# Performance work log

Measured on AMD Instinct MI355X. Metric: run time of the kernel, lower is better.

Reference implementation:

```python
import jax, jax.numpy as jnp
import numpy as np

INPUT_DIM = 1024
OUT_DIM = 1024
ORDER = 4
EXPANSION_POINT = 0.0


def setup_inputs() -> dict:
    key = jax.random.key(0)
    k_x, k_c = jax.random.split(key)
    x = jax.random.normal(k_x, (8192, INPUT_DIM), dtype=jnp.float32)
    coeffs = jax.random.normal(k_c, (OUT_DIM, INPUT_DIM, ORDER), dtype=jnp.float32) * 0.01
    bias = jnp.zeros((1, OUT_DIM), dtype=jnp.float32)
    return {"x": x, "coeffs": coeffs, "bias": bias}


def reference(x, coeffs, bias):
    # x: [..., input_dim] -> flatten leading dims
    outshape = x.shape[:-1] + (OUT_DIM,)
    xf = x.reshape(-1, INPUT_DIM)
    x_shifted = xf - EXPANSION_POINT
    # powers P[n, i, k] = x_shifted^k, k = 0..order-1 (0**0 == 1, matching torch)
    powers = jnp.power(x_shifted[:, :, None], jnp.arange(ORDER, dtype=x.dtype))
    # y[n, o] = sum_{i,k} P[n,i,k] * coeffs[o,i,k]  -- single GEMM-like contraction
    y = jnp.einsum('nik,oik->no', powers, coeffs)
    y = y + bias
    return y.reshape(outshape)
```

## Files before the change

kernel.cpp:

```cpp
#include <hip/hip_runtime.h>
#include <stdint.h>

#define IN_DIM 1024
#define OUT_DIM 1024
#define NROWS 8192
#define KD 3072

#define BM 256
#define BN 128
#define BK 64
#define NT (KD / BK)

typedef __bf16 bf16x8 __attribute__((ext_vector_type(8)));
typedef float f32x4 __attribute__((ext_vector_type(4)));
typedef unsigned short us8 __attribute__((ext_vector_type(8)));
typedef unsigned int u32;

#define AS1 __attribute__((address_space(1)))
#define AS3 __attribute__((address_space(3)))

__device__ __forceinline__ unsigned short f2bf(float f) {
    u32 u = __builtin_bit_cast(u32, f);
    u32 r = (u + 0x7fffu + ((u >> 16) & 1u)) >> 16;
    return (unsigned short)r;
}

__device__ __forceinline__ bf16x8 ld8(const unsigned short* p) {
    return __builtin_bit_cast(bf16x8, *reinterpret_cast<const us8*>(p));
}

__global__ __launch_bounds__(256) void prep_coeffs(const float* __restrict__ c,
                                                   const float* __restrict__ bias,
                                                   unsigned short* __restrict__ B,
                                                   float* __restrict__ bias2) {
    const int o = blockIdx.x;
    const float4* row = reinterpret_cast<const float4*>(c + (size_t)o * (IN_DIM * 4));
    unsigned short* Bo = B + (size_t)o * KD;
    float s = 0.f;
    for (int i = threadIdx.x; i < IN_DIM; i += 256) {
        float4 v = row[i];
        s += v.x;
        Bo[i]        = f2bf(v.y);
        Bo[1024 + i] = f2bf(v.z);
        Bo[2048 + i] = f2bf(v.w);
    }
#pragma unroll
    for (int off = 32; off; off >>= 1) s += __shfl_down(s, off);
    __shared__ float red[4];
    if ((threadIdx.x & 63) == 0) red[threadIdx.x >> 6] = s;
    __syncthreads();
    if (threadIdx.x == 0) bias2[o] = bias[o] + red[0] + red[1] + red[2] + red[3];
}

__global__ __launch_bounds__(256) void prep_powers(const float* __restrict__ x,
                                                   unsigned short* __restrict__ A) {
    int t = blockIdx.x * blockDim.x + threadIdx.x;
    int n = t >> 8;
    int i4 = (t & 255) * 4;
    float4 v = reinterpret_cast<const float4*>(x)[t];
    unsigned short* An = A + (size_t)n * KD + i4;
    float xs[4] = {v.x, v.y, v.z, v.w};
    unsigned short b1[4], b2[4], b3[4];
#pragma unroll
    for (int j = 0; j < 4; ++j) {
        float x1 = xs[j], x2 = x1 * x1, x3 = x2 * x1;
        b1[j] = f2bf(x1); b2[j] = f2bf(x2); b3[j] = f2bf(x3);
    }
    ushort4 p1 = {b1[0], b1[1], b1[2], b1[3]};
    ushort4 p2 = {b2[0], b2[1], b2[2], b2[3]};
    ushort4 p3 = {b3[0], b3[1], b3[2], b3[3]};
    *reinterpret_cast<ushort4*>(An)        = p1;
    *reinterpret_cast<ushort4*>(An + 1024) = p2;
    *reinterpret_cast<ushort4*>(An + 2048) = p3;
}

__global__ __launch_bounds__(512, 2) void taylor_gemm(
    const unsigned short* __restrict__ A,
    const unsigned short* __restrict__ B,
    const float* __restrict__ bias2,
    float* __restrict__ C) {
    __shared__ alignas(16) unsigned short sA[3][BM * BK];
    __shared__ alignas(16) unsigned short sB[3][BN * BK];

    const int tid = threadIdx.x;
    const int lane = tid & 63;
    const int wid = tid >> 6;
    const int wr = wid >> 1;
    const int wc = wid & 1;
    const int gx = blockIdx.x, gy = blockIdx.y;

    const char* Ab = (const char*)A;
    const char* Bb = (const char*)B;
    const int cs = ((lane & 7) ^ (lane >> 3)) * 8;
    size_t aSrc[4], bSrc[2];
    int aDst[4], bDst[2];
#pragma unroll
    for (int u = 0; u < 4; ++u) {
        int row = gx * BM + u * 64 + wid * 8 + (lane >> 3);
        aSrc[u] = ((size_t)row * KD + cs) * 2;
        aDst[u] = (u * 64 + wid * 8) * BK;
    }
#pragma unroll
    for (int u = 0; u < 2; ++u) {
        int row = gy * BN + u * 64 + wid * 8 + (lane >> 3);
        bSrc[u] = ((size_t)row * KD + cs) * 2;
        bDst[u] = (u * 64 + wid * 8) * BK;
    }

    auto stage_all = [&](int b, int kt) {
        size_t koff = (size_t)kt * (BK * 2);
#pragma unroll
        for (int u = 0; u < 4; ++u)
            __builtin_amdgcn_global_load_lds(
                (const AS1 void*)(Ab + aSrc[u] + koff),
                (AS3 void*)(&sA[b][aDst[u]]), 16, 0, 0);
#pragma unroll
        for (int u = 0; u < 2; ++u)
            __builtin_amdgcn_global_load_lds(
                (const AS1 void*)(Bb + bSrc[u] + koff),
                (AS3 void*)(&sB[b][bDst[u]]), 16, 0, 0);
    };

    int aSw[2], bSw[2];
#pragma unroll
    for (int ks = 0; ks < 2; ++ks) {
        int sw = ((ks * 4 + (lane >> 4)) ^ (lane & 7)) * 8;
        aSw[ks] = (wr * 64 + (lane & 15)) * BK + sw;
        bSw[ks] = (wc * 64 + (lane & 15)) * BK + sw;
    }

    bf16x8 fa0[4][2], fb0[4][2], fa1[4][2], fb1[4][2];
    f32x4 acc[4][4] = {};

    auto read_frags = [&](bf16x8 (&fa)[4][2], bf16x8 (&fb)[4][2], int b) {
        const unsigned short* sAc = &sA[b][0];
        const unsigned short* sBc = &sB[b][0];
#pragma unroll
        for (int n = 0; n < 4; ++n)
#pragma unroll
            for (int ks = 0; ks < 2; ++ks)
                fb[n][ks] = ld8(&sBc[bSw[ks] + n * 16 * BK]);
#pragma unroll
        for (int m = 0; m < 4; ++m)
#pragma unroll
            for (int ks = 0; ks < 2; ++ks)
                fa[m][ks] = ld8(&sAc[aSw[ks] + m * 16 * BK]);
    };

    auto mfma_all = [&](bf16x8 (&fa)[4][2], bf16x8 (&fb)[4][2]) {
        __builtin_amdgcn_s_setprio(1);
#pragma unroll
        for (int m = 0; m < 4; ++m)
#pragma unroll
            for (int n = 0; n < 4; ++n)
#pragma unroll
                for (int ks = 0; ks < 2; ++ks)
                    acc[m][n] = __builtin_amdgcn_mfma_f32_16x16x32_bf16(
                        fa[m][ks], fb[n][ks], acc[m][n], 0, 0, 0);
        __builtin_amdgcn_s_setprio(0);
    };

    stage_all(0, 0);
    stage_all(1, 1);
    asm volatile("s_waitcnt vmcnt(6)" ::: "memory");
    __builtin_amdgcn_s_barrier();
    __builtin_amdgcn_sched_barrier(0);
    read_frags(fa0, fb0, 0);

#define TAYLOR_ITER(kt, FAc, FBc, FAn, FBn)                                   \
    {                                                                         \
        asm volatile("s_waitcnt vmcnt(0)" ::: "memory");                      \
        __builtin_amdgcn_s_barrier();                                         \
        __builtin_amdgcn_sched_barrier(0);                                    \
        if ((kt) < NT - 2) stage_all(((kt) + 2) % 3, (kt) + 2);               \
        if ((kt) < NT - 1) read_frags(FAn, FBn, ((kt) + 1) % 3);              \
        __builtin_amdgcn_sched_barrier(0);                                    \
        mfma_all(FAc, FBc);                                                   \
    }

    for (int kt = 0; kt < NT; kt += 2) {
        TAYLOR_ITER(kt,     fa0, fb0, fa1, fb1);
        TAYLOR_ITER(kt + 1, fa1, fb1, fa0, fb0);
    }
#undef TAYLOR_ITER

    const int colBase = gy * BN + wc * 64 + (lane & 15);
    const int rowBase = gx * BM + wr * 64 + (lane >> 4) * 4;
#pragma unroll
    for (int n = 0; n < 4; ++n) {
        int col = colBase + n * 16;
        float bv = bias2[col];
#pragma unroll
        for (int m = 0; m < 4; ++m) {
            int row = rowBase + m * 16;
#pragma unroll
            for (int r = 0; r < 4; ++r)
                C[(size_t)(row + r) * OUT_DIM + col] = acc[m][n][r] + bv;
        }
    }
}

__global__ void taylor_naive(const float* __restrict__ x, const float* __restrict__ coeffs,
                             const float* __restrict__ bias, float* __restrict__ out) {
    int n = blockIdx.x;
    __shared__ float P[IN_DIM * 4];
    for (int i = threadIdx.x; i < IN_DIM; i += blockDim.x) {
        float xv = x[(size_t)n * IN_DIM + i];
        P[i * 4 + 0] = 1.f;
        P[i * 4 + 1] = xv;
        P[i * 4 + 2] = xv * xv;
        P[i * 4 + 3] = xv * xv * xv;
    }
    __syncthreads();
    for (int o = threadIdx.x; o < OUT_DIM; o += blockDim.x) {
        float s = bias[o];
        const float* c = coeffs + (size_t)o * (IN_DIM * 4);
        for (int i = 0; i < IN_DIM; ++i) {
            float4 cv = *reinterpret_cast<const float4*>(c + i * 4);
            s += cv.x * P[i * 4 + 0] + cv.y * P[i * 4 + 1] +
                 cv.z * P[i * 4 + 2] + cv.w * P[i * 4 + 3];
        }
        out[(size_t)n * OUT_DIM + o] = s;
    }
}

extern "C" void kernel_launch(void* const* d_in, const int* in_sizes, int n_in,
                              void* d_out, int out_size, void* d_ws, size_t ws_size,
                              hipStream_t stream) {
    const float* x = (const float*)d_in[0];
    const float* coeffs = (const float*)d_in[1];
    const float* bias = (const float*)d_in[2];
    float* out = (float*)d_out;

    const size_t needA = (size_t)NROWS * KD * 2;
    const size_t needB = (size_t)OUT_DIM * KD * 2;
    const size_t needBias = OUT_DIM * sizeof(float);

    if (ws_size >= needA + needB + needBias) {
        unsigned short* A = (unsigned short*)d_ws;
        unsigned short* B = (unsigned short*)((char*)d_ws + needA);
        float* bias2 = (float*)((char*)d_ws + needA + needB);
        prep_coeffs<<<OUT_DIM, 256, 0, stream>>>(coeffs, bias, B, bias2);
        prep_powers<<<(NROWS * IN_DIM / 4) / 256, 256, 0, stream>>>(x, A);
        dim3 grid(NROWS / BM, OUT_DIM / BN);
        taylor_gemm<<<grid, 512, 0, stream>>>(A, B, bias2, out);
    } else {
        taylor_naive<<<NROWS, 256, 0, stream>>>(x, coeffs, bias, out);
    }
}
```

Before: 87.91 us.

## Fuse power computation into GEMM, loading x directly into registers

Result: slower. 105.0 us (+19.5%).

```diff
diff --git a/kernel.cpp b/kernel.cpp
--- a/kernel.cpp
+++ b/kernel.cpp
@@ -8,8 +8,7 @@
 
 #define BM 256
 #define BN 128
-#define BK 64
-#define NT (KD / BK)
+#define NIC 16
 
 typedef __bf16 bf16x8 __attribute__((ext_vector_type(8)));
 typedef float f32x4 __attribute__((ext_vector_type(4)));
@@ -52,35 +51,12 @@
     if (threadIdx.x == 0) bias2[o] = bias[o] + red[0] + red[1] + red[2] + red[3];
 }
 
-__global__ __launch_bounds__(256) void prep_powers(const float* __restrict__ x,
-                                                   unsigned short* __restrict__ A) {
-    int t = blockIdx.x * blockDim.x + threadIdx.x;
-    int n = t >> 8;
-    int i4 = (t & 255) * 4;
-    float4 v = reinterpret_cast<const float4*>(x)[t];
-    unsigned short* An = A + (size_t)n * KD + i4;
-    float xs[4] = {v.x, v.y, v.z, v.w};
-    unsigned short b1[4], b2[4], b3[4];
-#pragma unroll
-    for (int j = 0; j < 4; ++j) {
-        float x1 = xs[j], x2 = x1 * x1, x3 = x2 * x1;
-        b1[j] = f2bf(x1); b2[j] = f2bf(x2); b3[j] = f2bf(x3);
-    }
-    ushort4 p1 = {b1[0], b1[1], b1[2], b1[3]};
-    ushort4 p2 = {b2[0], b2[1], b2[2], b2[3]};
-    ushort4 p3 = {b3[0], b3[1], b3[2], b3[3]};
-    *reinterpret_cast<ushort4*>(An)        = p1;
-    *reinterpret_cast<ushort4*>(An + 1024) = p2;
-    *reinterpret_cast<ushort4*>(An + 2048) = p3;
-}
-
 __global__ __launch_bounds__(512, 2) void taylor_gemm(
-    const unsigned short* __restrict__ A,
+    const float* __restrict__ x,
     const unsigned short* __restrict__ B,
     const float* __restrict__ bias2,
     float* __restrict__ C) {
-    __shared__ alignas(16) unsigned short sA[3][BM * BK];
-    __shared__ alignas(16) unsigned short sB[3][BN * BK];
+    __shared__ alignas(16) unsigned short sB[2][3][BN * 64];
 
     const int tid = threadIdx.x;
     const int lane = tid & 63;
@@ -89,100 +65,97 @@
     const int wc = wid & 1;
     const int gx = blockIdx.x, gy = blockIdx.y;
 
-    const char* Ab = (const char*)A;
     const char* Bb = (const char*)B;
     const int cs = ((lane & 7) ^ (lane >> 3)) * 8;
-    size_t aSrc[4], bSrc[2];
-    int aDst[4], bDst[2];
-#pragma unroll
-    for (int u = 0; u < 4; ++u) {
-        int row = gx * BM + u * 64 + wid * 8 + (lane >> 3);
-        aSrc[u] = ((size_t)row * KD + cs) * 2;
-        aDst[u] = (u * 64 + wid * 8) * BK;
-    }
+    size_t bSrc[2];
+    int bDst[2];
 #pragma unroll
     for (int u = 0; u < 2; ++u) {
         int row = gy * BN + u * 64 + wid * 8 + (lane >> 3);
         bSrc[u] = ((size_t)row * KD + cs) * 2;
-        bDst[u] = (u * 64 + wid * 8) * BK;
-    }
-
-    auto stage_all = [&](int b, int kt) {
-        size_t koff = (size_t)kt * (BK * 2);
-#pragma unroll
-        for (int u = 0; u < 4; ++u)
-            __builtin_amdgcn_global_load_lds(
-                (const AS1 void*)(Ab + aSrc[u] + koff),
-                (AS3 void*)(&sA[b][aDst[u]]), 16, 0, 0);
-#pragma unroll
-        for (int u = 0; u < 2; ++u)
-            __builtin_amdgcn_global_load_lds(
-                (const AS1 void*)(Bb + bSrc[u] + koff),
-                (AS3 void*)(&sB[b][bDst[u]]), 16, 0, 0);
+        bDst[u] = (u * 64 + wid * 8) * 64;
+    }
+
+    auto stage_all = [&](int d, int ic) {
+        size_t koff = (size_t)(ic * 64) * 2;
+#pragma unroll
+        for (int pp = 0; pp < 3; ++pp)
+#pragma unroll
+            for (int u = 0; u < 2; ++u)
+                __builtin_amdgcn_global_load_lds(
+                    (const AS1 void*)(Bb + bSrc[u] + (size_t)pp * 2048 + koff),
+                    (AS3 void*)(&sB[d][pp][bDst[u]]), 16, 0, 0);
     };
 
-    int aSw[2], bSw[2];
-#pragma unroll
-    for (int ks = 0; ks < 2; ++ks) {
-        int sw = ((ks * 4 + (lane >> 4)) ^ (lane & 7)) * 8;
-        aSw[ks] = (wr * 64 + (lane & 15)) * BK + sw;
-        bSw[ks] = (wc * 64 + (lane & 15)) * BK + sw;
-    }
-
-    bf16x8 fa0[4][2], fb0[4][2], fa1[4][2], fb1[4][2];
+    int bSw[2];
+#pragma unroll
+    for (int ks = 0; ks < 2; ++ks)
+        bSw[ks] = (wc * 64 + (lane & 15)) * 64 + (((ks * 4 + (lane >> 4)) ^ (lane & 7)) * 8);
+
+    const float* xb[4];
+#pragma unroll
+    for (int m = 0; m < 4; ++m)
+        xb[m] = x + (size_t)(gx * BM + wr * 64 + m * 16 + (lane & 15)) * IN_DIM
+                  + ((lane >> 4) * 8);
+
     f32x4 acc[4][4] = {};
 
-    auto read_frags = [&](bf16x8 (&fa)[4][2], bf16x8 (&fb)[4][2], int b) {
-        const unsigned short* sAc = &sA[b][0];
-        const unsigned short* sBc = &sB[b][0];
-#pragma unroll
-        for (int n = 0; n < 4; ++n)
-#pragma unroll
-            for (int ks = 0; ks < 2; ++ks)
-                fb[n][ks] = ld8(&sBc[bSw[ks] + n * 16 * BK]);
+    stage_all(0, 0);
+
+    for (int ic = 0; ic < NIC; ++ic) {
+        const int d = ic & 1;
+        asm volatile("s_waitcnt vmcnt(0)" ::: "memory");
+        __builtin_amdgcn_s_barrier();
+        __builtin_amdgcn_sched_barrier(0);
+        if (ic + 1 < NIC) stage_all(d ^ 1, ic + 1);
+
+        float4 xq[4][2][2];
 #pragma unroll
         for (int m = 0; m < 4; ++m)
 #pragma unroll
-            for (int ks = 0; ks < 2; ++ks)
-                fa[m][ks] = ld8(&sAc[aSw[ks] + m * 16 * BK]);
-    };
-
-    auto mfma_all = [&](bf16x8 (&fa)[4][2], bf16x8 (&fb)[4][2]) {
-        __builtin_amdgcn_s_setprio(1);
-#pragma unroll
-        for (int m = 0; m < 4; ++m)
+            for (int ks = 0; ks < 2; ++ks) {
+                const float* p = xb[m] + ic * 64 + ks * 32;
+                xq[m][ks][0] = *reinterpret_cast<const float4*>(p);
+                xq[m][ks][1] = *reinterpret_cast<const float4*>(p + 4);
+            }
+
+#pragma unroll
+        for (int pp = 0; pp < 3; ++pp) {
+            bf16x8 fb[4][2];
 #pragma unroll
             for (int n = 0; n < 4; ++n)
 #pragma unroll
                 for (int ks = 0; ks < 2; ++ks)
-                    acc[m][n] = __builtin_amdgcn_mfma_f32_16x16x32_bf16(
-                        fa[m][ks], fb[n][ks], acc[m][n], 0, 0, 0);
-        __builtin_amdgcn_s_setprio(0);
-    };
-
-    stage_all(0, 0);
-    stage_all(1, 1);
-    asm volatile("s_waitcnt vmcnt(6)" ::: "memory");
-    __builtin_amdgcn_s_barrier();
-    __builtin_amdgcn_sched_barrier(0);
-    read_frags(fa0, fb0, 0);
-
-#define TAYLOR_ITER(kt, FAc, FBc, FAn, FBn)                                   \
-    {                                                                         \
-        asm volatile("s_waitcnt vmcnt(0)" ::: "memory");                      \
-        __builtin_amdgcn_s_barrier();                                         \
-        __builtin_amdgcn_sched_barrier(0);                                    \
-        if ((kt) < NT - 2) stage_all(((kt) + 2) % 3, (kt) + 2);               \
-        if ((kt) < NT - 1) read_frags(FAn, FBn, ((kt) + 1) % 3);              \
-        __builtin_amdgcn_sched_barrier(0);                                    \
-        mfma_all(FAc, FBc);                                                   \
-    }
-
-    for (int kt = 0; kt < NT; kt += 2) {
-        TAYLOR_ITER(kt,     fa0, fb0, fa1, fb1);
-        TAYLOR_ITER(kt + 1, fa1, fb1, fa0, fb0);
-    }
-#undef TAYLOR_ITER
+                    fb[n][ks] = ld8(&sB[d][pp][bSw[ks] + n * 16 * 64]);
+
+#pragma unroll
+            for (int m = 0; m < 4; ++m) {
+                bf16x8 af[2];
+#pragma unroll
+                for (int ks = 0; ks < 2; ++ks) {
+                    float v[8] = {xq[m][ks][0].x, xq[m][ks][0].y,
+                                  xq[m][ks][0].z, xq[m][ks][0].w,
+                                  xq[m][ks][1].x, xq[m][ks][1].y,
+                                  xq[m][ks][1].z, xq[m][ks][1].w};
+#pragma unroll
+                    for (int j = 0; j < 8; ++j) {
+                        float w = v[j];
+                        if (pp >= 1) w *= v[j];
+                        if (pp == 2) w *= v[j];
+                        af[ks][j] = (__bf16)w;
+                    }
+                }
+                __builtin_amdgcn_s_setprio(1);
+#pragma unroll
+                for (int n = 0; n < 4; ++n)
+#pragma unroll
+                    for (int ks = 0; ks < 2; ++ks)
+                        acc[m][n] = __builtin_amdgcn_mfma_f32_16x16x32_bf16(
+                            af[ks], fb[n][ks], acc[m][n], 0, 0, 0);
+                __builtin_amdgcn_s_setprio(0);
+            }
+        }
+    }
 
     const int colBase = gy * BN + wc * 64 + (lane & 15);
     const int rowBase = gx * BM + wr * 64 + (lane >> 4) * 4;
@@ -232,18 +205,15 @@
     const float* bias = (const float*)d_in[2];
     float* out = (float*)d_out;
 
-    const size_t needA = (size_t)NROWS * KD * 2;
     const size_t needB = (size_t)OUT_DIM * KD * 2;
     const size_t needBias = OUT_DIM * sizeof(float);
 
-    if (ws_size >= needA + needB + needBias) {
-        unsigned short* A = (unsigned short*)d_ws;
-        unsigned short* B = (unsigned short*)((char*)d_ws + needA);
-        float* bias2 = (float*)((char*)d_ws + needA + needB);
+    if (ws_size >= needB + needBias) {
+        unsigned short* B = (unsigned short*)d_ws;
+        float* bias2 = (float*)((char*)d_ws + needB);
         prep_coeffs<<<OUT_DIM, 256, 0, stream>>>(coeffs, bias, B, bias2);
-        prep_powers<<<(NROWS * IN_DIM / 4) / 256, 256, 0, stream>>>(x, A);
         dim3 grid(NROWS / BM, OUT_DIM / BN);
-        taylor_gemm<<<grid, 512, 0, stream>>>(A, B, bias2, out);
+        taylor_gemm<<<grid, 512, 0, stream>>>(x, B, bias2, out);
     } else {
         taylor_naive<<<NROWS, 256, 0, stream>>>(x, coeffs, bias, out);
     }
```

## Shrink GEMM tile to 128x128 with 256 threads and double buffering

Applied to the files above, without the earlier changes.

Result: faster. 76.86 us (-12.6%).

```diff
diff --git a/kernel.cpp b/kernel.cpp
--- a/kernel.cpp
+++ b/kernel.cpp
@@ -6,7 +6,7 @@
 #define NROWS 8192
 #define KD 3072
 
-#define BM 256
+#define BM 128
 #define BN 128
 #define BK 64
 #define NT (KD / BK)
@@ -74,13 +74,13 @@
     *reinterpret_cast<ushort4*>(An + 2048) = p3;
 }
 
-__global__ __launch_bounds__(512, 2) void taylor_gemm(
+__global__ __launch_bounds__(256, 2) void taylor_gemm(
     const unsigned short* __restrict__ A,
     const unsigned short* __restrict__ B,
     const float* __restrict__ bias2,
     float* __restrict__ C) {
-    __shared__ alignas(16) unsigned short sA[3][BM * BK];
-    __shared__ alignas(16) unsigned short sB[3][BN * BK];
+    __shared__ alignas(16) unsigned short sA[2][BM * BK];
+    __shared__ alignas(16) unsigned short sB[2][BN * BK];
 
     const int tid = threadIdx.x;
     const int lane = tid & 63;
@@ -92,33 +92,28 @@
     const char* Ab = (const char*)A;
     const char* Bb = (const char*)B;
     const int cs = ((lane & 7) ^ (lane >> 3)) * 8;
-    size_t aSrc[4], bSrc[2];
-    int aDst[4], bDst[2];
+    size_t aSrc[4], bSrc[4];
+    int dstOff[4];
 #pragma unroll
     for (int u = 0; u < 4; ++u) {
-        int row = gx * BM + u * 64 + wid * 8 + (lane >> 3);
-        aSrc[u] = ((size_t)row * KD + cs) * 2;
-        aDst[u] = (u * 64 + wid * 8) * BK;
-    }
-#pragma unroll
-    for (int u = 0; u < 2; ++u) {
-        int row = gy * BN + u * 64 + wid * 8 + (lane >> 3);
-        bSrc[u] = ((size_t)row * KD + cs) * 2;
-        bDst[u] = (u * 64 + wid * 8) * BK;
-    }
-
-    auto stage_all = [&](int b, int kt) {
+        int row = u * 32 + wid * 8 + (lane >> 3);
+        aSrc[u] = ((size_t)(gx * BM + row) * KD + cs) * 2;
+        bSrc[u] = ((size_t)(gy * BN + row) * KD + cs) * 2;
+        dstOff[u] = row * BK - (lane >> 3) * BK;
+    }
+
+    auto stage_all = [&](int d, int kt) {
         size_t koff = (size_t)kt * (BK * 2);
 #pragma unroll
         for (int u = 0; u < 4; ++u)
             __builtin_amdgcn_global_load_lds(
                 (const AS1 void*)(Ab + aSrc[u] + koff),
-                (AS3 void*)(&sA[b][aDst[u]]), 16, 0, 0);
-#pragma unroll
-        for (int u = 0; u < 2; ++u)
+                (AS3 void*)(&sA[d][dstOff[u]]), 16, 0, 0);
+#pragma unroll
+        for (int u = 0; u < 4; ++u)
             __builtin_amdgcn_global_load_lds(
                 (const AS1 void*)(Bb + bSrc[u] + koff),
-                (AS3 void*)(&sB[b][bDst[u]]), 16, 0, 0);
+                (AS3 void*)(&sB[d][dstOff[u]]), 16, 0, 0);
     };
 
     int aSw[2], bSw[2];
@@ -129,26 +124,32 @@
         bSw[ks] = (wc * 64 + (lane & 15)) * BK + sw;
     }
 
-    bf16x8 fa0[4][2], fb0[4][2], fa1[4][2], fb1[4][2];
     f32x4 acc[4][4] = {};
 
-    auto read_frags = [&](bf16x8 (&fa)[4][2], bf16x8 (&fb)[4][2], int b) {
-        const unsigned short* sAc = &sA[b][0];
-        const unsigned short* sBc = &sB[b][0];
+    stage_all(0, 0);
+    asm volatile("s_waitcnt vmcnt(0)" ::: "memory");
+    __builtin_amdgcn_s_barrier();
+    __builtin_amdgcn_sched_barrier(0);
+
+    for (int kt = 0; kt < NT; ++kt) {
+        const int d = kt & 1;
+        const unsigned short* sAc = &sA[d][0];
+        const unsigned short* sBc = &sB[d][0];
+
+        bf16x8 af[4][2], bf[4][2];
+#pragma unroll
+        for (int m = 0; m < 4; ++m)
+#pragma unroll
+            for (int ks = 0; ks < 2; ++ks)
+                af[m][ks] = ld8(&sAc[aSw[ks] + m * 16 * BK]);
 #pragma unroll
         for (int n = 0; n < 4; ++n)
 #pragma unroll
             for (int ks = 0; ks < 2; ++ks)
-                fb[n][ks] = ld8(&sBc[bSw[ks] + n * 16 * BK]);
-#pragma unroll
-        for (int m = 0; m < 4; ++m)
-#pragma unroll
-            for (int ks = 0; ks < 2; ++ks)
-                fa[m][ks] = ld8(&sAc[aSw[ks] + m * 16 * BK]);
-    };
-
-    auto mfma_all = [&](bf16x8 (&fa)[4][2], bf16x8 (&fb)[4][2]) {
-        __builtin_amdgcn_s_setprio(1);
+                bf[n][ks] = ld8(&sBc[bSw[ks] + n * 16 * BK]);
+
+        if (kt + 1 < NT) stage_all(d ^ 1, kt + 1);
+
 #pragma unroll
         for (int m = 0; m < 4; ++m)
 #pragma unroll
@@ -156,33 +157,12 @@
 #pragma unroll
                 for (int ks = 0; ks < 2; ++ks)
                     acc[m][n] = __builtin_amdgcn_mfma_f32_16x16x32_bf16(
-                        fa[m][ks], fb[n][ks], acc[m][n], 0, 0, 0);
-        __builtin_amdgcn_s_setprio(0);
-    };
-
-    stage_all(0, 0);
-    stage_all(1, 1);
-    asm volatile("s_waitcnt vmcnt(6)" ::: "memory");
-    __builtin_amdgcn_s_barrier();
-    __builtin_amdgcn_sched_barrier(0);
-    read_frags(fa0, fb0, 0);
-
-#define TAYLOR_ITER(kt, FAc, FBc, FAn, FBn)                                   \
-    {                                                                         \
-        asm volatile("s_waitcnt vmcnt(0)" ::: "memory");                      \
-        __builtin_amdgcn_s_barrier();                                         \
-        __builtin_amdgcn_sched_barrier(0);                                    \
-        if ((kt) < NT - 2) stage_all(((kt) + 2) % 3, (kt) + 2);               \
-        if ((kt) < NT - 1) read_frags(FAn, FBn, ((kt) + 1) % 3);              \
-        __builtin_amdgcn_sched_barrier(0);                                    \
-        mfma_all(FAc, FBc);                                                   \
-    }
-
-    for (int kt = 0; kt < NT; kt += 2) {
-        TAYLOR_ITER(kt,     fa0, fb0, fa1, fb1);
-        TAYLOR_ITER(kt + 1, fa1, fb1, fa0, fb0);
-    }
-#undef TAYLOR_ITER
+                        af[m][ks], bf[n][ks], acc[m][n], 0, 0, 0);
+
+        asm volatile("s_waitcnt vmcnt(0)" ::: "memory");
+        __builtin_amdgcn_s_barrier();
+        __builtin_amdgcn_sched_barrier(0);
+    }
 
     const int colBase = gy * BN + wc * 64 + (lane & 15);
     const int rowBase = gx * BM + wr * 64 + (lane >> 4) * 4;
@@ -243,7 +223,7 @@
         prep_coeffs<<<OUT_DIM, 256, 0, stream>>>(coeffs, bias, B, bias2);
         prep_powers<<<(NROWS * IN_DIM / 4) / 256, 256, 0, stream>>>(x, A);
         dim3 grid(NROWS / BM, OUT_DIM / BN);
-        taylor_gemm<<<grid, 512, 0, stream>>>(A, B, bias2, out);
+        taylor_gemm<<<grid, 256, 0, stream>>>(A, B, bias2, out);
     } else {
         taylor_naive<<<NROWS, 256, 0, stream>>>(x, coeffs, bias, out);
     }
```
